# Kernel optimization log

Hardware: AMD Instinct MI355X
Metric: run time of the kernel (lower is better)

## Reference

```python
import jax, jax.numpy as jnp
import numpy as np

B, A, N, P = 1024, 25, 250, 250  # batch, NUM_AGENTS, graph_size, num patrol nodes


def setup_inputs() -> dict:
    key = jax.random.key(0)
    k1, k2, k3, k4 = jax.random.split(key, 4)
    state = jax.random.normal(k1, (B, A, N, 3), dtype=jnp.float32)
    nodes_coords = jax.random.normal(k2, (P, 2), dtype=jnp.float32)
    adj = jax.random.uniform(k3, (P, N), dtype=jnp.float32)
    node_last_visit = jax.random.randint(k4, (B, A), 0, P, dtype=jnp.int32)
    patrol_index = jnp.arange(P, dtype=jnp.int32)  # obsMap.patrol_nodes.index lookup table
    return {
        'state': state,
        'nodes_coords': nodes_coords,
        'adj': adj,
        'node_last_visit': node_last_visit,
        'patrol_index': patrol_index,
    }


def reference(state, nodes_coords, adj, node_last_visit, patrol_index):
    # Vectorized form of the nested per-(batch, agent) Python loops in Policy.forward:
    #   zuobiao[i, j] = obsMap.nodes[node_last_visit[i, j]]
    #   idx[i, j]     = patrol_nodes.index(node_last_visit[i, j])
    #   mask[i, j]    = adj[idx[i, j]]
    zuobiao = nodes_coords[node_last_visit]          # [B, A, 2]
    idx = patrol_index[node_last_visit]              # [B, A]
    mask = adj[idx]                                  # [B, A, N]
    # zuobiao broadcast over graph_size, then concat onto state (pads features 3 -> 5)
    zb = jnp.broadcast_to(zuobiao[:, :, None, :], (B, A, N, 2))
    state_cat = jnp.concatenate([state, zb], axis=-1)            # [B, A, N, 5]
    # Pack mask as an extra channel so the fused gather pipeline has one output.
    out = jnp.concatenate([state_cat, mask[..., None]], axis=-1)  # [B, A, N, 6]
    return out
```

## Files before the change

### kernel.cpp

```cpp
#include <hip/hip_runtime.h>
#include <hip/hip_bf16.h>

#define BB 1024
#define AA 25
#define NN 250
#define PP 250

__global__ __launch_bounds__(256) void policy_kernel(
    const float* __restrict__ state,
    const float* __restrict__ nodes_coords,
    const float* __restrict__ adj,
    const int*   __restrict__ nlv,
    const int*   __restrict__ patrol_index,
    float* __restrict__ out)
{
    __shared__ float s_state[NN * 3];
    __shared__ float s_adj[NN];

    const int ba  = blockIdx.x;
    const int tid = threadIdx.x;

    const int nv  = nlv[ba];
    const int idx = patrol_index[nv];
    const float zx = nodes_coords[2 * nv + 0];
    const float zy = nodes_coords[2 * nv + 1];

    const float* st = state + (size_t)ba * (NN * 3);
    const float* ad = adj   + (size_t)idx * NN;

    {
        const float2* st2 = (const float2*)st;
        float2* ss2 = (float2*)s_state;
        for (int i = tid; i < (NN * 3) / 2; i += 256)
            ss2[i] = st2[i];
    }
    if (tid < NN) s_adj[tid] = ad[tid];
    __syncthreads();

    float* op = out + (size_t)ba * (NN * 6);
    float4* op4 = (float4*)op;

    for (int q = tid; q < (NN * 6) / 4; q += 256) {
        const int g  = q / 3;
        const int r  = q - 3 * g;
        const int n0 = 2 * g;
        const int sb = 3 * n0;
        float4 v;
        if (r == 0) {
            v.x = s_state[sb + 0];
            v.y = s_state[sb + 1];
            v.z = s_state[sb + 2];
            v.w = zx;
        } else if (r == 1) {
            v.x = zy;
            v.y = s_adj[n0];
            v.z = s_state[sb + 3];
            v.w = s_state[sb + 4];
        } else {
            v.x = s_state[sb + 5];
            v.y = zx;
            v.z = zy;
            v.w = s_adj[n0 + 1];
        }
        op4[q] = v;
    }
}

extern "C" void kernel_launch(void* const* d_in, const int* in_sizes, int n_in,
                              void* d_out, int out_size, void* d_ws, size_t ws_size,
                              hipStream_t stream) {
    const float* state        = (const float*)d_in[0];
    const float* nodes_coords = (const float*)d_in[1];
    const float* adj          = (const float*)d_in[2];
    const int*   nlv          = (const int*)d_in[3];
    const int*   patrol_index = (const int*)d_in[4];
    float* out = (float*)d_out;

    policy_kernel<<<dim3(BB * AA), dim3(256), 0, stream>>>(
        state, nodes_coords, adj, nlv, patrol_index, out);
}
```

Measured before the change: 223.4 us.

## Map one wave per batch-agent row with direct register gather and nontemporal I/O

Replaces the one-block-per-row kernel, which staged data through shared memory and synchronized, with a grid-stride scheme where each 64-lane wave handles one (batch, agent) row. Each lane loads three float2 state pieces and one float2 adjacency pair, assembles three float4 outputs in registers, and writes them with nontemporal stores. Uniform indices are moved to scalar registers via readfirstlane. The aim is to drop LDS traffic, barriers and per-element branching, and to cut launch overhead for this bandwidth-bound copy. The cost is that state loads become 8-byte strided accesses and some lanes sit idle, since 125 groups do not fill two full waves.

```diff
diff --git a/kernel.cpp b/kernel.cpp
--- a/kernel.cpp
+++ b/kernel.cpp
@@ -1,12 +1,18 @@
 #include <hip/hip_runtime.h>
-#include <hip/hip_bf16.h>
 
 #define BB 1024
 #define AA 25
 #define NN 250
 #define PP 250
+#define BA (BB * AA)
+#define GROUPS 125
+#define BLOCKS 1600
+#define TPB 256
 
-__global__ __launch_bounds__(256) void policy_kernel(
+typedef float v2f __attribute__((ext_vector_type(2)));
+typedef float v4f __attribute__((ext_vector_type(4)));
+
+__global__ __launch_bounds__(TPB) void policy_kernel(
     const float* __restrict__ state,
     const float* __restrict__ nodes_coords,
     const float* __restrict__ adj,
@@ -14,55 +20,35 @@
     const int*   __restrict__ patrol_index,
     float* __restrict__ out)
 {
-    __shared__ float s_state[NN * 3];
-    __shared__ float s_adj[NN];
+    const int tid    = threadIdx.x;
+    const int lane   = tid & 63;
+    const int wave   = (blockIdx.x << 2) | (tid >> 6);
+    const int nwaves = BLOCKS << 2;
 
-    const int ba  = blockIdx.x;
-    const int tid = threadIdx.x;
+    for (int ba = wave; ba < BA; ba += nwaves) {
+        const int nv  = __builtin_amdgcn_readfirstlane(nlv[ba]);
+        const int idx = __builtin_amdgcn_readfirstlane(patrol_index[nv]);
+        const float zx = nodes_coords[2 * nv + 0];
+        const float zy = nodes_coords[2 * nv + 1];
 
-    const int nv  = nlv[ba];
-    const int idx = patrol_index[nv];
-    const float zx = nodes_coords[2 * nv + 0];
-    const float zy = nodes_coords[2 * nv + 1];
+        const v2f* st2 = (const v2f*)(state + (size_t)ba * (NN * 3));
+        const v2f* ad2 = (const v2f*)(adj + (size_t)idx * NN);
+        v4f* op4 = (v4f*)(out + (size_t)ba * (NN * 6));
 
-    const float* st = state + (size_t)ba * (NN * 3);
-    const float* ad = adj   + (size_t)idx * NN;
+        for (int g = lane; g < GROUPS; g += 64) {
+            v2f s0 = __builtin_nontemporal_load(&st2[3 * g + 0]);
+            v2f s1 = __builtin_nontemporal_load(&st2[3 * g + 1]);
+            v2f s2 = __builtin_nontemporal_load(&st2[3 * g + 2]);
+            v2f a  = ad2[g];
 
-    {
-        const float2* st2 = (const float2*)st;
-        float2* ss2 = (float2*)s_state;
-        for (int i = tid; i < (NN * 3) / 2; i += 256)
-            ss2[i] = st2[i];
-    }
-    if (tid < NN) s_adj[tid] = ad[tid];
-    __syncthreads();
+            v4f v0 = {s0.x, s0.y, s1.x, zx};
+            v4f v1 = {zy, a.x, s1.y, s2.x};
+            v4f v2 = {s2.y, zx, zy, a.y};
 
-    float* op = out + (size_t)ba * (NN * 6);
-    float4* op4 = (float4*)op;
-
-    for (int q = tid; q < (NN * 6) / 4; q += 256) {
-        const int g  = q / 3;
-        const int r  = q - 3 * g;
-        const int n0 = 2 * g;
-        const int sb = 3 * n0;
-        float4 v;
-        if (r == 0) {
-            v.x = s_state[sb + 0];
-            v.y = s_state[sb + 1];
-            v.z = s_state[sb + 2];
-            v.w = zx;
-        } else if (r == 1) {
-            v.x = zy;
-            v.y = s_adj[n0];
-            v.z = s_state[sb + 3];
-            v.w = s_state[sb + 4];
-        } else {
-            v.x = s_state[sb + 5];
-            v.y = zx;
-            v.z = zy;
-            v.w = s_adj[n0 + 1];
+            __builtin_nontemporal_store(v0, &op4[3 * g + 0]);
+            __builtin_nontemporal_store(v1, &op4[3 * g + 1]);
+            __builtin_nontemporal_store(v2, &op4[3 * g + 2]);
         }
-        op4[q] = v;
     }
 }
 
@@ -76,6 +62,6 @@
     const int*   patrol_index = (const int*)d_in[4];
     float* out = (float*)d_out;
 
-    policy_kernel<<<dim3(BB * AA), dim3(256), 0, stream>>>(
+    policy_kernel<<<dim3(BLOCKS), dim3(TPB), 0, stream>>>(
         state, nodes_coords, adj, nlv, patrol_index, out);
 }
```

New measurement: 243.3 us. 8.9% more time.
